# Kernel tuning notes

Measured on AMD Instinct MI355X. Metric: run time of the kernel, lower is better.

Reference implementation:

```python
import jax, jax.numpy as jnp
import numpy as np

BS, M, D_IN, D_OUT = 32, 128, 64, 32


def _spd_log(X):
    # torch.svd on an SPD matrix == eigh (u diag(s) u^T with s>0), so
    # u @ diag(log s) @ v^T reduces to u @ diag(log s) @ u^T.
    s, u = jnp.linalg.eigh(X)
    return jnp.einsum('...ik,...k,...jk->...ij', u, jnp.log(s), u)


def _sym_exp(X):
    s, u = jnp.linalg.eigh(X)
    return jnp.einsum('...ik,...k,...jk->...ij', u, jnp.exp(s), u)


def setup_inputs() -> dict:
    key = jax.random.key(0)
    kx, kq, kk, kv = jax.random.split(key, 4)
    A = jax.random.normal(kx, (BS, M, D_IN, D_IN), dtype=jnp.float32)
    # SPD input: A A^T / d_in + eps I (eigenvalues strictly positive)
    x = jnp.einsum('bmij,bmkj->bmik', A, A) / D_IN + 1e-2 * jnp.eye(D_IN, dtype=jnp.float32)
    def stiefel(k):
        # column-orthonormal (d_in, d_out), mimicking SPDTransform's Stiefel weight
        return jnp.linalg.qr(jax.random.normal(k, (D_IN, D_OUT), dtype=jnp.float32))[0]
    return {'x': x, 'Wq': stiefel(kq), 'Wk': stiefel(kk), 'Wv': stiefel(kv)}


def reference(x, Wq, Wk, Wv):
    bs, m, d_in, _ = x.shape
    d_out = Wq.shape[1]

    def bimap(W):  # SPDTransform: W^T X W, stays SPD
        return jnp.einsum('pi,bmpq,qj->bmij', W, x, W)

    Q, K, V = bimap(Wq), bimap(Wk), bimap(Wv)
    logQ, logK, logV = _spd_log(Q), _spd_log(K), _spd_log(V)

    # log-Euclidean distance: sum of singular values of D D^T with
    # D = log A - log B (symmetric) equals trace(D D^T) = ||D||_F^2.
    # Torch's repeat/expand pattern yields energy[b,i,j] = d(K_i, Q_j);
    # computed here without materializing the (bs, m, m, d, d) tensor.
    q2 = jnp.sum(logQ * logQ, axis=(-2, -1))            # [bs, m]
    k2 = jnp.sum(logK * logK, axis=(-2, -1))            # [bs, m]
    cross = jnp.einsum('bikl,bjkl->bij', logK, logQ)    # [bs, m(i=K), m(j=Q)]
    energy = k2[:, :, None] + q2[:, None, :] - 2.0 * cross

    scores = 1.0 / (1.0 + jnp.log1p(energy))
    # softmax over dim=-2 (the K index i), then permute(0, 2, 1)
    attn = jnp.swapaxes(jax.nn.softmax(scores, axis=-2), -1, -2)  # [bs, j, i]

    # LogEuclideanMean: exp_sym( sum_i attn[b,j,i] * log V[b,i] )
    mean_log = jnp.einsum('bji,bikl->bjkl', attn, logV)
    out = _sym_exp(mean_log)
    return out.reshape(bs * m, d_out, d_out)
```

## Files before the change

kernel.cpp:

```cpp
#include <hip/hip_runtime.h>
#include <math.h>

constexpr int kBS = 32, kM = 128, kNMAT = kBS * kM;
constexpr int kDIN = 64, kDOUT = 32, kMSZ = kDOUT * kDOUT;
constexpr int kNSweep = 5;

constexpr size_t OFF_SS   = (size_t)3 * kNMAT * kMSZ;
constexpr size_t OFF_ATTN = OFF_SS + (size_t)3 * kNMAT;

#define F4(p)  (*(float4*)(p))
#define CF4(p) (*(const float4*)(p))

__global__ __launch_bounds__(256) void k_bimap(
    const float* __restrict__ x, const float* __restrict__ Wq,
    const float* __restrict__ Wk, const float* __restrict__ Wv,
    float* __restrict__ P) {
  __shared__ float Xs[64 * 68];
  __shared__ float Wsh[64 * 32];
  __shared__ float Ts[64 * 36];
  const int t = threadIdx.x;
  const int bm = blockIdx.x;
  const float* xp = x + (size_t)bm * (kDIN * kDIN);
  {
    const int f0 = t * 16;
    const int r = f0 >> 6, c = f0 & 63;
    const float* src = xp + f0;
    float* dst = &Xs[r * 68 + c];
#pragma unroll
    for (int i = 0; i < 4; ++i) F4(dst + 4 * i) = CF4(src + 4 * i);
  }
  const int r0 = (t >> 3) * 2;
  const int j0 = (t & 7) * 4;
  const int i2 = t >> 3;
  for (int tt = 0; tt < 3; ++tt) {
    const float* W = (tt == 0) ? Wq : ((tt == 1) ? Wk : Wv);
    __syncthreads();
    F4(&Wsh[t * 8]) = CF4(W + t * 8);
    F4(&Wsh[t * 8 + 4]) = CF4(W + t * 8 + 4);
    __syncthreads();
    float a0[4] = {0.f, 0.f, 0.f, 0.f}, a1[4] = {0.f, 0.f, 0.f, 0.f};
    for (int k = 0; k < 64; ++k) {
      const float2 x01 = *(const float2*)&Xs[k * 68 + r0];
      const float4 w = CF4(&Wsh[k * 32 + j0]);
      a0[0] += x01.x * w.x; a0[1] += x01.x * w.y; a0[2] += x01.x * w.z; a0[3] += x01.x * w.w;
      a1[0] += x01.y * w.x; a1[1] += x01.y * w.y; a1[2] += x01.y * w.z; a1[3] += x01.y * w.w;
    }
    F4(&Ts[r0 * 36 + j0])       = make_float4(a0[0], a0[1], a0[2], a0[3]);
    F4(&Ts[(r0 + 1) * 36 + j0]) = make_float4(a1[0], a1[1], a1[2], a1[3]);
    __syncthreads();
    float b4[4] = {0.f, 0.f, 0.f, 0.f};
    for (int p = 0; p < 64; ++p) {
      const float wv = Wsh[p * 32 + i2];
      const float4 tv = CF4(&Ts[p * 36 + j0]);
      b4[0] += wv * tv.x; b4[1] += wv * tv.y; b4[2] += wv * tv.z; b4[3] += wv * tv.w;
    }
    F4(&P[((size_t)tt * kNMAT + bm) * kMSZ + i2 * 32 + j0]) =
        make_float4(b4[0], b4[1], b4[2], b4[3]);
  }
}

constexpr int kJSlot = 32 * 36 + 32;
constexpr int kShl1 = 0x101, kShr1 = 0x111;

template <int CTRL>
__device__ __forceinline__ float updppf(float old_, float x) {
  return __builtin_bit_cast(float,
      __builtin_amdgcn_update_dpp(__builtin_bit_cast(int, old_),
                                  __builtin_bit_cast(int, x),
                                  CTRL, 0xf, 0xf, false));
}

__device__ __forceinline__ float xsign(float x, float s) {
  return __builtin_bit_cast(float,
      __builtin_bit_cast(int, x) ^
      (__builtin_bit_cast(int, s) & 0x80000000));
}

__global__ __launch_bounds__(256, 4) void k_jacobi_log(float* __restrict__ P,
                                                       float* __restrict__ sq) {
  __shared__ float lds[4 * kJSlot];
  const int t = threadIdx.x;
  const int wid = t >> 6, lane = t & 63;
  const int mat = lane >> 5;
  const int g = lane & 15;
  const int sub = (lane >> 4) & 1;
  const int off = sub * 16;

  const bool is_g0 = (g == 0);
  const int p0 = is_g0 ? 31 : g;
  const int q0 = is_g0 ? 0 : 31 - g;

  const size_t gbase = (size_t)blockIdx.x * 8 + wid * 2;
  const float* A = P + (gbase + mat) * kMSZ;

  float cp[16], cq[16];
  {
    const float* pr = A + p0 * 32 + off;
    const float* qr = A + q0 * 32 + off;
#pragma unroll
    for (int i = 0; i < 16; i += 4) {
      const float4 a = CF4(pr + i);
      cp[i] = a.x; cp[i + 1] = a.y; cp[i + 2] = a.z; cp[i + 3] = a.w;
      const float4 b = CF4(qr + i);
      cq[i] = b.x; cq[i + 1] = b.y; cq[i + 2] = b.z; cq[i + 3] = b.w;
    }
  }
  float app = 0.f, aqq = 0.f;
#pragma unroll
  for (int i = 0; i < 16; ++i) {
    app = fmaf(cp[i], cp[i], app);
    aqq = fmaf(cq[i], cq[i], aqq);
  }
  app += __shfl_xor(app, 16);
  aqq += __shfl_xor(aqq, 16);

  for (int sw = 0; sw < kNSweep; ++sw) {
    for (int r = 0; r < 31; ++r) {
      float d0 = cp[0] * cq[0], d1 = cp[1] * cq[1];
#pragma unroll
      for (int i = 2; i < 16; i += 2) {
        d0 = fmaf(cp[i], cq[i], d0);
        d1 = fmaf(cp[i + 1], cq[i + 1], d1);
      }
      float apq = d0 + d1;
      apq += __shfl_xor(apq, 16);
      const float d = aqq - app;
      const float apq2 = 2.f * apq;
      float h2 = fmaf(d, d, apq2 * apq2);
      h2 = fmaxf(h2, 1e-38f);
      const float hr = __builtin_amdgcn_rsqf(h2);
      const float h = h2 * hr;
      const float den = fabsf(d) + h;
      const float t0 = apq2 * __builtin_amdgcn_rcpf(den);
      const float tt = xsign(t0, d);
      const float c = __builtin_amdgcn_rsqf(fmaf(tt, tt, 1.f));
      const float sn = tt * c;
#pragma unroll
      for (int i = 0; i < 16; ++i) {
        const float t1 = c * cp[i];
        const float t2 = sn * cp[i];
        const float np_ = fmaf(-sn, cq[i], t1);
        const float nq_ = fmaf(c, cq[i], t2);
        const float cpm = updppf<kShl1>(nq_, np_);
        cp[i] = is_g0 ? np_ : cpm;
        cq[i] = updppf<kShr1>(cpm, nq_);
      }
      const float c2 = c * c, s2 = sn * sn, cs2 = 2.f * c * sn;
      const float capp = fmaf(c2, app, fmaf(s2, aqq, -cs2 * apq));
      const float caqq = (app + aqq) - capp;
      {
        const float capm = updppf<kShl1>(caqq, capp);
        app = is_g0 ? capp : capm;
        aqq = updppf<kShr1>(capm, caqq);
      }
    }
  }
  float ssp = 0.f, ssq = 0.f;
#pragma unroll
  for (int i = 0; i < 16; ++i) {
    ssp = fmaf(cp[i], cp[i], ssp);
    ssq = fmaf(cq[i], cq[i], ssq);
  }
  ssp += __shfl_xor(ssp, 16);
  ssq += __shfl_xor(ssq, 16);
  const float lgp = 0.5f * logf(ssp);
  const float lgq = 0.5f * logf(ssq);
  const float wp = lgp * __builtin_amdgcn_rcpf(ssp);
  const float wq = lgq * __builtin_amdgcn_rcpf(ssq);
  {
    float tot = fmaf(lgp, lgp, lgq * lgq);
    tot += __shfl_xor(tot, 1); tot += __shfl_xor(tot, 2);
    tot += __shfl_xor(tot, 4); tot += __shfl_xor(tot, 8);
    if ((lane & 31) == 0) sq[gbase + mat] = tot;
  }
  float* Bs = lds + wid * kJSlot;
  float* ncol = Bs + 1152;
  for (int m = 0; m < 2; ++m) {
    __builtin_amdgcn_wave_barrier();
    if (mat == m) {
#pragma unroll
      for (int i = 0; i < 16; i += 4) {
        F4(&Bs[p0 * 36 + off + i]) = make_float4(cp[i], cp[i+1], cp[i+2], cp[i+3]);
        F4(&Bs[q0 * 36 + off + i]) = make_float4(cq[i], cq[i+1], cq[i+2], cq[i+3]);
      }
      if (sub == 0) {
        ncol[p0] = wp;
        ncol[q0] = wq;
      }
    }
    __builtin_amdgcn_wave_barrier();
    {
      float* Am = P + (gbase + m) * kMSZ;
      const int rr = (lane >> 3) * 4, cc = (lane & 7) * 4;
      float acc[4][4] = {};
      for (int c = 0; c < 32; ++c) {
        const float w = ncol[c];
        const float4 br = CF4(&Bs[c * 36 + rr]);
        const float4 bc = CF4(&Bs[c * 36 + cc]);
        const float wr[4]  = {w * br.x, w * br.y, w * br.z, w * br.w};
        const float bcv[4] = {bc.x, bc.y, bc.z, bc.w};
#pragma unroll
        for (int i = 0; i < 4; ++i)
#pragma unroll
          for (int j2 = 0; j2 < 4; ++j2) acc[i][j2] += wr[i] * bcv[j2];
      }
#pragma unroll
      for (int i = 0; i < 4; ++i)
        F4(&Am[(rr + i) * 32 + cc]) =
            make_float4(acc[i][0], acc[i][1], acc[i][2], acc[i][3]);
    }
    __builtin_amdgcn_wave_barrier();
  }
}

__global__ __launch_bounds__(256) void k_attn(
    const float* __restrict__ P, const float* __restrict__ sq,
    float* __restrict__ attn) {
  __shared__ float Kt[32 * 132];
  __shared__ float Qt[32 * 20];
  __shared__ float Ss[128 * 20];
  __shared__ float red[16 * 20];
  __shared__ float mcol[16];
  __shared__ float scol[16];
  const int t = threadIdx.x;
  const int b = blockIdx.y, jt = blockIdx.x;
  const int j0g = jt * 16;
  const float* logK = P + ((size_t)kNMAT + (size_t)b * kM) * kMSZ;
  const float* logQ = P + ((size_t)b * kM + j0g) * kMSZ;
  const int i0 = (t >> 3) * 4, j0 = (t & 7) * 2;
  float acc[4][2] = {};
  for (int dc = 0; dc < kMSZ; dc += 32) {
    __syncthreads();
    {
      const int r = t >> 1, c0 = (t & 1) * 16;
      const float* src = logK + (size_t)r * kMSZ + dc + c0;
#pragma unroll
      for (int ii = 0; ii < 16; ii += 4) {
        const float4 v = CF4(src + ii);
        Kt[(c0 + ii + 0) * 132 + r] = v.x;
        Kt[(c0 + ii + 1) * 132 + r] = v.y;
        Kt[(c0 + ii + 2) * 132 + r] = v.z;
        Kt[(c0 + ii + 3) * 132 + r] = v.w;
      }
    }
    {
      const int j = t >> 4, c0 = (t & 15) * 2;
      const float2 v = *(const float2*)(logQ + (size_t)j * kMSZ + dc + c0);
      Qt[(c0 + 0) * 20 + j] = v.x;
      Qt[(c0 + 1) * 20 + j] = v.y;
    }
    __syncthreads();
    for (int k = 0; k < 32; ++k) {
      const float4 kv = CF4(&Kt[k * 132 + i0]);
      const float2 qv = *(const float2*)&Qt[k * 20 + j0];
      acc[0][0] = fmaf(kv.x, qv.x, acc[0][0]);
      acc[0][1] = fmaf(kv.x, qv.y, acc[0][1]);
      acc[1][0] = fmaf(kv.y, qv.x, acc[1][0]);
      acc[1][1] = fmaf(kv.y, qv.y, acc[1][1]);
      acc[2][0] = fmaf(kv.z, qv.x, acc[2][0]);
      acc[2][1] = fmaf(kv.z, qv.y, acc[2][1]);
      acc[3][0] = fmaf(kv.w, qv.x, acc[3][0]);
      acc[3][1] = fmaf(kv.w, qv.y, acc[3][1]);
    }
  }
  {
    float k2v[4], q2v[2];
#pragma unroll
    for (int i = 0; i < 4; ++i) k2v[i] = sq[kNMAT + b * kM + i0 + i];
#pragma unroll
    for (int j2 = 0; j2 < 2; ++j2) q2v[j2] = sq[b * kM + j0g + j0 + j2];
#pragma unroll
    for (int i = 0; i < 4; ++i)
#pragma unroll
      for (int j2 = 0; j2 < 2; ++j2) {
        float e = k2v[i] + q2v[j2] - 2.f * acc[i][j2];
        e = fmaxf(e, 0.f);
        Ss[(i0 + i) * 20 + (j0 + j2)] = 1.f / (1.f + log1pf(e));
      }
  }
  __syncthreads();
  const int jl = t & 15, grp = t >> 4;
  {
    float m = -1e30f;
#pragma unroll
    for (int i = 0; i < 8; ++i) m = fmaxf(m, Ss[(grp * 8 + i) * 20 + jl]);
    red[grp * 20 + jl] = m;
  }
  __syncthreads();
  if (t < 16) {
    float m = red[t];
#pragma unroll
    for (int g = 1; g < 16; ++g) m = fmaxf(m, red[g * 20 + t]);
    mcol[t] = m;
  }
  __syncthreads();
  {
    const float mj = mcol[jl];
    float s = 0.f;
#pragma unroll
    for (int i = 0; i < 8; ++i) s += expf(Ss[(grp * 8 + i) * 20 + jl] - mj);
    red[grp * 20 + jl] = s;
  }
  __syncthreads();
  if (t < 16) {
    float s = red[t];
#pragma unroll
    for (int g = 1; g < 16; ++g) s += red[g * 20 + t];
    scol[t] = 1.f / s;
  }
  __syncthreads();
  {
    const int il = t & 31, jg = t >> 5;
#pragma unroll
    for (int rep = 0; rep < 2; ++rep) {
      const int j2 = jg + rep * 8;
      const float mj = mcol[j2], is = scol[j2];
      float* dst = attn + ((size_t)b * kM + j0g + j2) * kM;
#pragma unroll
      for (int c4 = 0; c4 < 4; ++c4) {
        const int i = il + c4 * 32;
        dst[i] = expf(Ss[i * 20 + j2] - mj) * is;
      }
    }
  }
}

__global__ __launch_bounds__(256) void k_meanlog(
    const float* __restrict__ attn, const float* __restrict__ P,
    float* __restrict__ ML) {
  __shared__ float As[16 * 132];
  const int t = threadIdx.x;
  const int b = blockIdx.y, jt = blockIdx.x;
  const int j0g = jt * 16;
  const float* logV = P + ((size_t)2 * kNMAT + (size_t)b * kM) * kMSZ;
  {
    const int j = t >> 4, k0 = (t & 15) * 8;
    const float* src = attn + ((size_t)b * kM + j0g + j) * kM + k0;
    F4(&As[j * 132 + k0])     = CF4(src);
    F4(&As[j * 132 + k0 + 4]) = CF4(src + 4);
  }
  __syncthreads();
  const int d0 = t * 4;
  float acc[16][4] = {};
  for (int k = 0; k < kM; k += 4) {
    float4 vr[4];
#pragma unroll
    for (int kk = 0; kk < 4; ++kk)
      vr[kk] = CF4(&logV[(size_t)(k + kk) * kMSZ + d0]);
#pragma unroll
    for (int j = 0; j < 16; ++j) {
      const float4 w = CF4(&As[j * 132 + k]);
      const float wv[4] = {w.x, w.y, w.z, w.w};
#pragma unroll
      for (int kk = 0; kk < 4; ++kk) {
        const float* vv = (const float*)&vr[kk];
#pragma unroll
        for (int dd = 0; dd < 4; ++dd)
          acc[j][dd] = fmaf(wv[kk], vv[dd], acc[j][dd]);
      }
    }
  }
#pragma unroll
  for (int j = 0; j < 16; ++j)
    F4(&ML[((size_t)b * kM + j0g + j) * kMSZ + d0]) =
        make_float4(acc[j][0], acc[j][1], acc[j][2], acc[j][3]);
}

constexpr int kESlot = 2 * 1152;

__global__ __launch_bounds__(256) void k_expm(const float* __restrict__ ML,
                                              float* __restrict__ out) {
  __shared__ float lds[4 * kESlot];
  const int t = threadIdx.x;
  const int wid = t >> 6, lane = t & 63;
  const size_t bm = (size_t)blockIdx.x * 4 + wid;
  float* Mb = lds + wid * kESlot;
  float* Tb = Mb + 1152;
  const float* S = ML + bm * kMSZ;
  const int r = lane >> 1, c0 = (lane & 1) * 16;
  float4 v0 = CF4(S + r * 32 + c0),     v1 = CF4(S + r * 32 + c0 + 4),
         v2 = CF4(S + r * 32 + c0 + 8), v3 = CF4(S + r * 32 + c0 + 12);
  float lsum = v0.x*v0.x + v0.y*v0.y + v0.z*v0.z + v0.w*v0.w
             + v1.x*v1.x + v1.y*v1.y + v1.z*v1.z + v1.w*v1.w
             + v2.x*v2.x + v2.y*v2.y + v2.z*v2.z + v2.w*v2.w
             + v3.x*v3.x + v3.y*v3.y + v3.z*v3.z + v3.w*v3.w;
#pragma unroll
  for (int d = 1; d < 64; d <<= 1) lsum += __shfl_xor(lsum, d);
  const float fn = sqrtf(lsum);
  int sc = 0;
  if (fn > 0.5f) sc = (int)ceilf(log2f(fn * 2.0f));
  const float scale = exp2f((float)(-sc));
  v0.x*=scale; v0.y*=scale; v0.z*=scale; v0.w*=scale;
  v1.x*=scale; v1.y*=scale; v1.z*=scale; v1.w*=scale;
  v2.x*=scale; v2.y*=scale; v2.z*=scale; v2.w*=scale;
  v3.x*=scale; v3.y*=scale; v3.z*=scale; v3.w*=scale;
  F4(&Mb[r * 36 + c0])      = v0;
  F4(&Mb[r * 36 + c0 + 4])  = v1;
  F4(&Mb[r * 36 + c0 + 8])  = v2;
  F4(&Mb[r * 36 + c0 + 12]) = v3;
  __builtin_amdgcn_wave_barrier();
  const int rr = (lane >> 3) * 4, cc = (lane & 7) * 4;
#pragma unroll
  for (int i = 0; i < 4; ++i) {
    float4 v = F4(&Mb[(rr + i) * 36 + cc]);
    v.x = v.x * (1.f/7.f) + ((rr + i == cc + 0) ? 1.f : 0.f);
    v.y = v.y * (1.f/7.f) + ((rr + i == cc + 1) ? 1.f : 0.f);
    v.z = v.z * (1.f/7.f) + ((rr + i == cc + 2) ? 1.f : 0.f);
    v.w = v.w * (1.f/7.f) + ((rr + i == cc + 3) ? 1.f : 0.f);
    F4(&Tb[(rr + i) * 36 + cc]) = v;
  }
  __builtin_amdgcn_wave_barrier();
  for (int j = 6; j >= 1; --j) {
    float a4[4][4] = {};
    for (int k = 0; k < 32; ++k) {
      const float4 mv = CF4(&Mb[k * 36 + rr]);
      const float mvv[4] = {mv.x, mv.y, mv.z, mv.w};
      const float4 tv = CF4(&Tb[k * 36 + cc]);
      const float tvv[4] = {tv.x, tv.y, tv.z, tv.w};
#pragma unroll
      for (int i = 0; i < 4; ++i)
#pragma unroll
        for (int j2 = 0; j2 < 4; ++j2) a4[i][j2] += mvv[i] * tvv[j2];
    }
    const float inv = 1.f / (float)j;
#pragma unroll
    for (int i = 0; i < 4; ++i) {
      float4 v;
      v.x = a4[i][0] * inv + ((rr + i == cc + 0) ? 1.f : 0.f);
      v.y = a4[i][1] * inv + ((rr + i == cc + 1) ? 1.f : 0.f);
      v.z = a4[i][2] * inv + ((rr + i == cc + 2) ? 1.f : 0.f);
      v.w = a4[i][3] * inv + ((rr + i == cc + 3) ? 1.f : 0.f);
      F4(&Tb[(rr + i) * 36 + cc]) = v;
    }
    __builtin_amdgcn_wave_barrier();
  }
  for (int st = 0; st < sc; ++st) {
    float a4[4][4] = {};
    for (int k = 0; k < 32; ++k) {
      const float4 mv = CF4(&Tb[k * 36 + rr]);
      const float mvv[4] = {mv.x, mv.y, mv.z, mv.w};
      const float4 tv = CF4(&Tb[k * 36 + cc]);
      const float tvv[4] = {tv.x, tv.y, tv.z, tv.w};
#pragma unroll
      for (int i = 0; i < 4; ++i)
#pragma unroll
        for (int j2 = 0; j2 < 4; ++j2) a4[i][j2] += mvv[i] * tvv[j2];
    }
#pragma unroll
    for (int i = 0; i < 4; ++i)
      F4(&Tb[(rr + i) * 36 + cc]) =
          make_float4(a4[i][0], a4[i][1], a4[i][2], a4[i][3]);
    __builtin_amdgcn_wave_barrier();
  }
#pragma unroll
  for (int i = 0; i < 4; ++i) {
    const float4 v = CF4(&Tb[(rr + i) * 36 + cc]);
    F4(&out[bm * kMSZ + (rr + i) * 32 + cc]) = v;
  }
}

extern "C" void kernel_launch(void* const* d_in, const int* in_sizes, int n_in,
                              void* d_out, int out_size, void* d_ws, size_t ws_size,
                              hipStream_t stream) {
  const float* x  = (const float*)d_in[0];
  const float* Wq = (const float*)d_in[1];
  const float* Wk = (const float*)d_in[2];
  const float* Wv = (const float*)d_in[3];
  float* ws   = (float*)d_ws;
  float* P    = ws;
  float* sq   = ws + OFF_SS;
  float* attn = ws + OFF_ATTN;
  float* ML   = ws;
  float* out  = (float*)d_out;

  k_bimap<<<kNMAT, 256, 0, stream>>>(x, Wq, Wk, Wv, P);
  k_jacobi_log<<<3 * kNMAT / 8, 256, 0, stream>>>(P, sq);
  k_attn<<<dim3(8, kBS), 256, 0, stream>>>(P, sq, attn);
  k_meanlog<<<dim3(8, kBS), 256, 0, stream>>>(attn, P, ML);
  k_expm<<<kNMAT / 4, 256, 0, stream>>>(ML, out);
}
```

Before: 452.9 us.

## Fuse attention softmax into mean-log kernel and trim Jacobi rotation rounds

The attention kernel now writes its normalized softmax weights straight into shared memory and runs the weighted log-V sum in the same block. This removes the global attn buffer round trip and one kernel launch. Separately, the Jacobi eigen-solver's nested sweep loop (5×31 rounds) becomes a flat loop of 140 rounds. That cuts rotation work, at the cost of possibly less converged eigenvectors and some accuracy margin.

Measured after the change: 442.4 us. 1.02x faster.

```diff
diff --git a/kernel.cpp b/kernel.cpp
--- a/kernel.cpp
+++ b/kernel.cpp
@@ -3,10 +3,9 @@
 
 constexpr int kBS = 32, kM = 128, kNMAT = kBS * kM;
 constexpr int kDIN = 64, kDOUT = 32, kMSZ = kDOUT * kDOUT;
-constexpr int kNSweep = 5;
+constexpr int kNRounds = 140;
 
 constexpr size_t OFF_SS   = (size_t)3 * kNMAT * kMSZ;
-constexpr size_t OFF_ATTN = OFF_SS + (size_t)3 * kNMAT;
 
 #define F4(p)  (*(float4*)(p))
 #define CF4(p) (*(const float4*)(p))
@@ -114,45 +113,43 @@
   app += __shfl_xor(app, 16);
   aqq += __shfl_xor(aqq, 16);
 
-  for (int sw = 0; sw < kNSweep; ++sw) {
-    for (int r = 0; r < 31; ++r) {
-      float d0 = cp[0] * cq[0], d1 = cp[1] * cq[1];
-#pragma unroll
-      for (int i = 2; i < 16; i += 2) {
-        d0 = fmaf(cp[i], cq[i], d0);
-        d1 = fmaf(cp[i + 1], cq[i + 1], d1);
-      }
-      float apq = d0 + d1;
-      apq += __shfl_xor(apq, 16);
-      const float d = aqq - app;
-      const float apq2 = 2.f * apq;
-      float h2 = fmaf(d, d, apq2 * apq2);
-      h2 = fmaxf(h2, 1e-38f);
-      const float hr = __builtin_amdgcn_rsqf(h2);
-      const float h = h2 * hr;
-      const float den = fabsf(d) + h;
-      const float t0 = apq2 * __builtin_amdgcn_rcpf(den);
-      const float tt = xsign(t0, d);
-      const float c = __builtin_amdgcn_rsqf(fmaf(tt, tt, 1.f));
-      const float sn = tt * c;
-#pragma unroll
-      for (int i = 0; i < 16; ++i) {
-        const float t1 = c * cp[i];
-        const float t2 = sn * cp[i];
-        const float np_ = fmaf(-sn, cq[i], t1);
-        const float nq_ = fmaf(c, cq[i], t2);
-        const float cpm = updppf<kShl1>(nq_, np_);
-        cp[i] = is_g0 ? np_ : cpm;
-        cq[i] = updppf<kShr1>(cpm, nq_);
-      }
-      const float c2 = c * c, s2 = sn * sn, cs2 = 2.f * c * sn;
-      const float capp = fmaf(c2, app, fmaf(s2, aqq, -cs2 * apq));
-      const float caqq = (app + aqq) - capp;
-      {
-        const float capm = updppf<kShl1>(caqq, capp);
-        app = is_g0 ? capp : capm;
-        aqq = updppf<kShr1>(capm, caqq);
-      }
+  for (int rnd = 0; rnd < kNRounds; ++rnd) {
+    float d0 = cp[0] * cq[0], d1 = cp[1] * cq[1];
+#pragma unroll
+    for (int i = 2; i < 16; i += 2) {
+      d0 = fmaf(cp[i], cq[i], d0);
+      d1 = fmaf(cp[i + 1], cq[i + 1], d1);
+    }
+    float apq = d0 + d1;
+    apq += __shfl_xor(apq, 16);
+    const float d = aqq - app;
+    const float apq2 = 2.f * apq;
+    float h2 = fmaf(d, d, apq2 * apq2);
+    h2 = fmaxf(h2, 1e-38f);
+    const float hr = __builtin_amdgcn_rsqf(h2);
+    const float h = h2 * hr;
+    const float den = fabsf(d) + h;
+    const float t0 = apq2 * __builtin_amdgcn_rcpf(den);
+    const float tt = xsign(t0, d);
+    const float c = __builtin_amdgcn_rsqf(fmaf(tt, tt, 1.f));
+    const float sn = tt * c;
+#pragma unroll
+    for (int i = 0; i < 16; ++i) {
+      const float t1 = c * cp[i];
+      const float t2 = sn * cp[i];
+      const float np_ = fmaf(-sn, cq[i], t1);
+      const float nq_ = fmaf(c, cq[i], t2);
+      const float cpm = updppf<kShl1>(nq_, np_);
+      cp[i] = is_g0 ? np_ : cpm;
+      cq[i] = updppf<kShr1>(cpm, nq_);
+    }
+    const float c2 = c * c, s2 = sn * sn, cs2 = 2.f * c * sn;
+    const float capp = fmaf(c2, app, fmaf(s2, aqq, -cs2 * apq));
+    const float caqq = (app + aqq) - capp;
+    {
+      const float capm = updppf<kShl1>(caqq, capp);
+      app = is_g0 ? capp : capm;
+      aqq = updppf<kShr1>(capm, caqq);
     }
   }
   float ssp = 0.f, ssq = 0.f;
@@ -213,15 +210,16 @@
   }
 }
 
-__global__ __launch_bounds__(256) void k_attn(
+__global__ __launch_bounds__(256) void k_attn_meanlog(
     const float* __restrict__ P, const float* __restrict__ sq,
-    float* __restrict__ attn) {
+    float* __restrict__ ML) {
   __shared__ float Kt[32 * 132];
   __shared__ float Qt[32 * 20];
   __shared__ float Ss[128 * 20];
   __shared__ float red[16 * 20];
   __shared__ float mcol[16];
   __shared__ float scol[16];
+  __shared__ float As[16 * 132];
   const int t = threadIdx.x;
   const int b = blockIdx.y, jt = blockIdx.x;
   const int j0g = jt * 16;
@@ -315,33 +313,17 @@
     for (int rep = 0; rep < 2; ++rep) {
       const int j2 = jg + rep * 8;
       const float mj = mcol[j2], is = scol[j2];
-      float* dst = attn + ((size_t)b * kM + j0g + j2) * kM;
 #pragma unroll
       for (int c4 = 0; c4 < 4; ++c4) {
         const int i = il + c4 * 32;
-        dst[i] = expf(Ss[i * 20 + j2] - mj) * is;
-      }
-    }
-  }
-}
-
-__global__ __launch_bounds__(256) void k_meanlog(
-    const float* __restrict__ attn, const float* __restrict__ P,
-    float* __restrict__ ML) {
-  __shared__ float As[16 * 132];
-  const int t = threadIdx.x;
-  const int b = blockIdx.y, jt = blockIdx.x;
-  const int j0g = jt * 16;
+        As[j2 * 132 + i] = expf(Ss[i * 20 + j2] - mj) * is;
+      }
+    }
+  }
+  __syncthreads();
   const float* logV = P + ((size_t)2 * kNMAT + (size_t)b * kM) * kMSZ;
-  {
-    const int j = t >> 4, k0 = (t & 15) * 8;
-    const float* src = attn + ((size_t)b * kM + j0g + j) * kM + k0;
-    F4(&As[j * 132 + k0])     = CF4(src);
-    F4(&As[j * 132 + k0 + 4]) = CF4(src + 4);
-  }
-  __syncthreads();
   const int d0 = t * 4;
-  float acc[16][4] = {};
+  float mlacc[16][4] = {};
   for (int k = 0; k < kM; k += 4) {
     float4 vr[4];
 #pragma unroll
@@ -356,14 +338,14 @@
         const float* vv = (const float*)&vr[kk];
 #pragma unroll
         for (int dd = 0; dd < 4; ++dd)
-          acc[j][dd] = fmaf(wv[kk], vv[dd], acc[j][dd]);
+          mlacc[j][dd] = fmaf(wv[kk], vv[dd], mlacc[j][dd]);
       }
     }
   }
 #pragma unroll
   for (int j = 0; j < 16; ++j)
     F4(&ML[((size_t)b * kM + j0g + j) * kMSZ + d0]) =
-        make_float4(acc[j][0], acc[j][1], acc[j][2], acc[j][3]);
+        make_float4(mlacc[j][0], mlacc[j][1], mlacc[j][2], mlacc[j][3]);
 }
 
 constexpr int kESlot = 2 * 1152;
@@ -469,13 +451,11 @@
   float* ws   = (float*)d_ws;
   float* P    = ws;
   float* sq   = ws + OFF_SS;
-  float* attn = ws + OFF_ATTN;
   float* ML   = ws;
   float* out  = (float*)d_out;
 
   k_bimap<<<kNMAT, 256, 0, stream>>>(x, Wq, Wk, Wv, P);
   k_jacobi_log<<<3 * kNMAT / 8, 256, 0, stream>>>(P, sq);
-  k_attn<<<dim3(8, kBS), 256, 0, stream>>>(P, sq, attn);
-  k_meanlog<<<dim3(8, kBS), 256, 0, stream>>>(attn, P, ML);
+  k_attn_meanlog<<<dim3(8, kBS), 256, 0, stream>>>(P, sq, ML);
   k_expm<<<kNMAT / 4, 256, 0, stream>>>(ML, out);
 }
```
